# Kernel tuning notes

Measured on AMD Instinct MI355X. Metric: run time of the kernel, lower is better.

Reference implementation:

```python
import jax, jax.numpy as jnp
import numpy as np

EMBED = 1024
HEADS = 16
HEAD_DIM = 64
FF = 4096
EPS = 1e-5


def _layernorm(x, g, b):
    mu = jnp.mean(x, axis=-1, keepdims=True)
    var = jnp.mean(jnp.square(x - mu), axis=-1, keepdims=True)
    return (x - mu) * jax.lax.rsqrt(var + EPS) * g + b


def setup_inputs() -> dict:
    key = jax.random.key(0)
    ks = jax.random.split(key, 12)
    s_in = 1.0 / np.sqrt(EMBED)
    s_hd = 1.0 / np.sqrt(HEADS * HEAD_DIM)
    s_ff = 1.0 / np.sqrt(FF)
    return {
        "x": jax.random.normal(ks[0], (4, 2048, EMBED), dtype=jnp.float32),
        "Wq": jax.random.uniform(ks[1], (HEADS, EMBED, HEAD_DIM), jnp.float32, -s_in, s_in),
        "Wk": jax.random.uniform(ks[2], (HEADS, EMBED, HEAD_DIM), jnp.float32, -s_in, s_in),
        "Wv": jax.random.uniform(ks[3], (HEADS, EMBED, HEAD_DIM), jnp.float32, -s_in, s_in),
        "Wo": jax.random.uniform(ks[4], (HEADS * HEAD_DIM, EMBED), jnp.float32, -s_hd, s_hd),
        "bo": jax.random.uniform(ks[5], (EMBED,), jnp.float32, -s_hd, s_hd),
        "W1": jax.random.uniform(ks[6], (EMBED, FF), jnp.float32, -s_in, s_in),
        "b1": jax.random.uniform(ks[7], (FF,), jnp.float32, -s_in, s_in),
        "W2": jax.random.uniform(ks[8], (FF, EMBED), jnp.float32, -s_ff, s_ff),
        "b2": jax.random.uniform(ks[9], (EMBED,), jnp.float32, -s_ff, s_ff),
        "ln1_g": jnp.ones((EMBED,), jnp.float32),
        "ln1_b": jnp.zeros((EMBED,), jnp.float32),
        "ln2_g": jnp.ones((EMBED,), jnp.float32),
        "ln2_b": jnp.zeros((EMBED,), jnp.float32),
    }


def reference(x, Wq, Wk, Wv, Wo, bo, W1, b1, W2, b2, ln1_g, ln1_b, ln2_g, ln2_b):
    B, T, C = x.shape
    h = _layernorm(x, ln1_g, ln1_b)
    # per-head projections, batched over heads: [B,H,T,Dh]
    q = jnp.einsum("btc,hcd->bhtd", h, Wq)
    k = jnp.einsum("btc,hcd->bhtd", h, Wk)
    v = jnp.einsum("btc,hcd->bhtd", h, Wv)
    scale = HEAD_DIM ** -0.5
    att = jnp.einsum("bhtd,bhsd->bhts", q, k) * scale  # [B,H,T,T]
    causal = jnp.tril(jnp.ones((T, T), dtype=bool))
    att = jnp.where(causal, att, -jnp.inf)
    att = jax.nn.softmax(att, axis=-1)
    out = jnp.einsum("bhts,bhsd->bhtd", att, v)  # [B,H,T,Dh]
    # concat heads (matches torch.cat over head outputs) -> [B,T,H*Dh]
    out = out.transpose(0, 2, 1, 3).reshape(B, T, HEADS * HEAD_DIM)
    x = x + out @ Wo + bo
    h2 = _layernorm(x, ln2_g, ln2_b)
    ff = jax.nn.relu(h2 @ W1 + b1) @ W2 + b2
    return x + ff
```

## Files before the change

### kernel.cpp

```cpp
#include <hip/hip_runtime.h>
#include <hip/hip_bf16.h>

#define EMBED 1024
#define HEADS 16
#define HEAD_DIM 64
#define FFDIM 4096
#define TSEQ 2048
#define BATCH 4
#define ROWS (BATCH * TSEQ)

typedef __bf16 bf16;
typedef __attribute__((ext_vector_type(8))) __bf16 bf16x8;
typedef __attribute__((ext_vector_type(4))) __bf16 bf16x4;
typedef __attribute__((ext_vector_type(4))) float f32x4;

typedef const __attribute__((address_space(1))) void* gvp;
typedef __attribute__((address_space(3))) void* svp;

__global__ __launch_bounds__(256) void conv_wqkv_t(
    const float* __restrict__ Wq, const float* __restrict__ Wk,
    const float* __restrict__ Wv, bf16* __restrict__ WqkvT) {
  __shared__ bf16 t[64][72];
  int tid = threadIdx.x;
  int k0 = blockIdx.x * 64;
  int head = blockIdx.y;
  int which = blockIdx.z;
  const float* src = which == 0 ? Wq : which == 1 ? Wk : Wv;
  float scale = which == 0 ? 0.125f * 1.44269504088896f : 1.0f;
  src += (size_t)head * 65536;
  bf16* dst = WqkvT + ((size_t)which * 1024 + head * 64) * 1024;
#pragma unroll
  for (int i = 0; i < 4; ++i) {
    int r = i * 16 + (tid >> 4);
    int c = (tid & 15) * 4;
    float4 v = *(const float4*)&src[(size_t)(k0 + r) * 64 + c];
    t[c + 0][r] = (bf16)(v.x * scale);
    t[c + 1][r] = (bf16)(v.y * scale);
    t[c + 2][r] = (bf16)(v.z * scale);
    t[c + 3][r] = (bf16)(v.w * scale);
  }
  __syncthreads();
#pragma unroll
  for (int i = 0; i < 2; ++i) {
    int r = i * 32 + (tid >> 3);
    int c = (tid & 7) * 8;
    bf16x8 o;
#pragma unroll
    for (int j = 0; j < 8; ++j) o[j] = t[r][c + j];
    *(bf16x8*)&dst[(size_t)r * 1024 + k0 + c] = o;
  }
}

__global__ __launch_bounds__(256) void transpose_conv(
    const float* __restrict__ W, bf16* __restrict__ WT, int K, int N) {
  __shared__ bf16 t[64][72];
  int tid = threadIdx.x;
  int n0 = blockIdx.x * 64, k0 = blockIdx.y * 64;
#pragma unroll
  for (int i = 0; i < 4; ++i) {
    int r = i * 16 + (tid >> 4);
    int c = (tid & 15) * 4;
    float4 v = *(const float4*)&W[(size_t)(k0 + r) * N + n0 + c];
    t[c + 0][r] = (bf16)v.x;
    t[c + 1][r] = (bf16)v.y;
    t[c + 2][r] = (bf16)v.z;
    t[c + 3][r] = (bf16)v.w;
  }
  __syncthreads();
#pragma unroll
  for (int i = 0; i < 2; ++i) {
    int r = i * 32 + (tid >> 3);
    int c = (tid & 7) * 8;
    bf16x8 o;
#pragma unroll
    for (int j = 0; j < 8; ++j) o[j] = t[r][c + j];
    *(bf16x8*)&WT[(size_t)(n0 + r) * K + k0 + c] = o;
  }
}

__global__ __launch_bounds__(256) void transpose_v(const bf16* __restrict__ v,
                                                   bf16* __restrict__ vt) {
  __shared__ bf16 t[64][72];
  int bh = blockIdx.y;
  int t0 = blockIdx.x * 64;
  const bf16* src = v + (size_t)bh * 131072;
  bf16* dst = vt + (size_t)bh * 131072;
  int tid = threadIdx.x;
#pragma unroll
  for (int i = 0; i < 2; ++i) {
    int c = tid + i * 256;
    int r = c >> 3, d0 = (c & 7) * 8;
    bf16x8 vv = *(const bf16x8*)&src[(size_t)(t0 + r) * 64 + d0];
#pragma unroll
    for (int j = 0; j < 8; ++j) t[d0 + j][r] = vv[j];
  }
  __syncthreads();
#pragma unroll
  for (int i = 0; i < 2; ++i) {
    int c = tid + i * 256;
    int r = c >> 3, s0 = (c & 7) * 8;
    bf16x8 o;
#pragma unroll
    for (int j = 0; j < 8; ++j) o[j] = t[r][s0 + j];
    *(bf16x8*)&dst[(size_t)r * 2048 + t0 + s0] = o;
  }
}

__global__ __launch_bounds__(256) void ln_kernel(
    const float* __restrict__ x, const float* __restrict__ g,
    const float* __restrict__ bta, bf16* __restrict__ out) {
  int row = blockIdx.x;
  const float* xr = x + (size_t)row * EMBED;
  float4 v = ((const float4*)xr)[threadIdx.x];
  float s1 = v.x + v.y + v.z + v.w;
  float s2 = v.x * v.x + v.y * v.y + v.z * v.z + v.w * v.w;
#pragma unroll
  for (int off = 1; off < 64; off <<= 1) {
    s1 += __shfl_xor(s1, off);
    s2 += __shfl_xor(s2, off);
  }
  __shared__ float red[8];
  int wid = threadIdx.x >> 6;
  int lane = threadIdx.x & 63;
  if (lane == 0) {
    red[wid * 2] = s1;
    red[wid * 2 + 1] = s2;
  }
  __syncthreads();
  s1 = red[0] + red[2] + red[4] + red[6];
  s2 = red[1] + red[3] + red[5] + red[7];
  float mu = s1 * (1.0f / EMBED);
  float var = s2 * (1.0f / EMBED) - mu * mu;
  float rs = rsqrtf(var + 1e-5f);
  float4 gv = ((const float4*)g)[threadIdx.x];
  float4 bv = ((const float4*)bta)[threadIdx.x];
  bf16x4 o;
  o[0] = (bf16)((v.x - mu) * rs * gv.x + bv.x);
  o[1] = (bf16)((v.y - mu) * rs * gv.y + bv.y);
  o[2] = (bf16)((v.z - mu) * rs * gv.z + bv.z);
  o[3] = (bf16)((v.w - mu) * rs * gv.w + bv.w);
  *(bf16x4*)(out + (size_t)row * EMBED + threadIdx.x * 4) = o;
}

template <int EPI>
__global__ __launch_bounds__(512, 1) void gemm256(
    const bf16* __restrict__ A, const bf16* __restrict__ BT,
    bf16* __restrict__ Cb, const float* __restrict__ bias, int M, int N,
    int K) {
  __shared__ __attribute__((aligned(16))) char lds[98304];
  int gx = gridDim.x;
  int nwg = gx * gridDim.y;
  int wgid = blockIdx.y * gx + blockIdx.x;
  int cpx = nwg >> 3;
  int swz = (wgid & 7) * cpx + (wgid >> 3);
  int m0 = (swz / gx) * 256, n0 = (swz % gx) * 256;
  int tid = threadIdx.x;
  int lane = tid & 63, wid = tid >> 6;
  int lr = lane & 15, lg = lane >> 4;
  int wrM = (wid >> 2) * 128;
  int wcN = (wid & 3) * 64;
  int crow = lane >> 2;
  int slotg = (lane & 3) ^ (crow & 3);
  int NT = K >> 5;
  size_t rb = (size_t)K * 2;

  auto stageA = [&](int t) {
    char* dst = lds + ((unsigned)t % 3u) * 32768u;
#pragma unroll
    for (int q = 0; q < 2; ++q) {
      int c = wid * 2 + q;
      const char* srcA = (const char*)A + (size_t)(m0 + c * 16 + crow) * rb +
                         (size_t)t * 64 + slotg * 16;
      __builtin_amdgcn_global_load_lds((gvp)srcA, (svp)(dst + c * 1024), 16, 0,
                                       0);
    }
  };
  auto stageB = [&](int t) {
    char* dst = lds + ((unsigned)t % 3u) * 32768u + 16384u;
#pragma unroll
    for (int q = 0; q < 2; ++q) {
      int c = wid * 2 + q;
      const char* srcB = (const char*)BT + (size_t)(n0 + c * 16 + crow) * rb +
                         (size_t)t * 64 + slotg * 16;
      __builtin_amdgcn_global_load_lds((gvp)srcB, (svp)(dst + c * 1024), 16, 0,
                                       0);
    }
  };

  stageA(0);
  stageB(0);
  stageA(1);
  stageB(1);
  f32x4 acc[8][4] = {};
  int swcol = ((lg ^ (lr & 3)) * 16);
  for (int t = 0; t < NT; ++t) {
    if (t == NT - 1)
      asm volatile("s_waitcnt vmcnt(0)" ::: "memory");
    else
      asm volatile("s_waitcnt vmcnt(4)" ::: "memory");
    __builtin_amdgcn_s_barrier();
    __builtin_amdgcn_sched_barrier(0);
    const char* Ab = lds + ((unsigned)t % 3u) * 32768u;
    const char* Bb = Ab + 16384;
    int tn = t + 2;
    bool st = tn < NT;
    bf16x8 bfr[4], afA[4], afB[4];
#pragma unroll
    for (int j = 0; j < 4; ++j)
      bfr[j] = *(const bf16x8*)(Bb + (wcN + j * 16 + lr) * 64 + swcol);
#pragma unroll
    for (int i = 0; i < 4; ++i)
      afA[i] = *(const bf16x8*)(Ab + (wrM + i * 16 + lr) * 64 + swcol);
    if (st) stageA(tn);
    __builtin_amdgcn_s_barrier();
    __builtin_amdgcn_sched_barrier(0);
    __builtin_amdgcn_s_setprio(1);
#pragma unroll
    for (int i = 0; i < 4; ++i)
#pragma unroll
      for (int j = 0; j < 4; ++j)
        acc[i][j] = __builtin_amdgcn_mfma_f32_16x16x32_bf16(afA[i], bfr[j],
                                                            acc[i][j], 0, 0, 0);
    __builtin_amdgcn_s_setprio(0);
    __builtin_amdgcn_sched_barrier(0);
#pragma unroll
    for (int i = 0; i < 4; ++i)
      afB[i] = *(const bf16x8*)(Ab + (wrM + 64 + i * 16 + lr) * 64 + swcol);
    if (st) stageB(tn);
    __builtin_amdgcn_s_barrier();
    __builtin_amdgcn_sched_barrier(0);
    __builtin_amdgcn_s_setprio(1);
#pragma unroll
    for (int i = 0; i < 4; ++i)
#pragma unroll
      for (int j = 0; j < 4; ++j)
        acc[4 + i][j] = __builtin_amdgcn_mfma_f32_16x16x32_bf16(
            afB[i], bfr[j], acc[4 + i][j], 0, 0, 0);
    __builtin_amdgcn_s_setprio(0);
    __builtin_amdgcn_sched_barrier(0);
  }
#pragma unroll
  for (int i = 0; i < 8; ++i) {
#pragma unroll
    for (int j = 0; j < 4; ++j) {
#pragma unroll
      for (int r = 0; r < 4; ++r) {
        int row = m0 + wrM + i * 16 + lg * 4 + r;
        int col = n0 + wcN + j * 16 + lr;
        float v = acc[i][j][r];
        if (EPI == 0) {
          int which = col >> 10, cc = col & 1023;
          int b = row >> 11, tt = row & 2047, h = cc >> 6, d = cc & 63;
          bf16* dst = Cb + (size_t)which * 8388608;
          dst[((size_t)((b << 4) + h) * TSEQ + tt) * HEAD_DIM + d] = (bf16)v;
        } else {
          size_t o = (size_t)row * N + col;
          float u = v + bias[col];
          Cb[o] = (bf16)(u > 0.f ? u : 0.f);
        }
      }
    }
  }
}

template <int EPI>
__global__ __launch_bounds__(256) void gemm_bf16(
    const bf16* __restrict__ A, const bf16* __restrict__ BT,
    float* __restrict__ Cf, bf16* __restrict__ Cb,
    const float* __restrict__ bias, const float* __restrict__ resid, int M,
    int N, int K) {
  __shared__ __attribute__((aligned(16))) bf16 As[128 * 32];
  __shared__ __attribute__((aligned(16))) bf16 Bs[128 * 32];
  int gx = gridDim.x;
  int nwg = gx * gridDim.y;
  int wgid = blockIdx.y * gx + blockIdx.x;
  int cpx = nwg >> 3;
  int swz = (wgid & 7) * cpx + (wgid >> 3);
  int m0 = (swz / gx) * 128, n0 = (swz % gx) * 128;
  int tid = threadIdx.x;
  int lane = tid & 63, wid = tid >> 6;
  int lr = lane & 15, lg = lane >> 4;
  int wr = (wid >> 1) * 64, wc = (wid & 1) * 64;
  int srow = lane >> 2;
  int sk = (lane & 3) * 8;
  f32x4 acc[4][4] = {};
  for (int kt = 0; kt < K; kt += 32) {
#pragma unroll
    for (int i = 0; i < 2; ++i) {
      int c = wid * 2 + i;
      int row = c * 16 + srow;
      const bf16* ga = &A[(size_t)(m0 + row) * K + kt + sk];
      const bf16* gb = &BT[(size_t)(n0 + row) * K + kt + sk];
      __builtin_amdgcn_global_load_lds((gvp)(const void*)ga,
                                       (svp)(void*)&As[c * 512], 16, 0, 0);
      __builtin_amdgcn_global_load_lds((gvp)(const void*)gb,
                                       (svp)(void*)&Bs[c * 512], 16, 0, 0);
    }
    __syncthreads();
    bf16x8 af[4], bfr[4];
#pragma unroll
    for (int i = 0; i < 4; ++i) {
      af[i] = *(const bf16x8*)&As[(wr + i * 16 + lr) * 32 + lg * 8];
      bfr[i] = *(const bf16x8*)&Bs[(wc + i * 16 + lr) * 32 + lg * 8];
    }
#pragma unroll
    for (int ar = 0; ar < 4; ++ar)
#pragma unroll
      for (int br = 0; br < 4; ++br)
        acc[ar][br] = __builtin_amdgcn_mfma_f32_16x16x32_bf16(
            af[ar], bfr[br], acc[ar][br], 0, 0, 0);
    __syncthreads();
  }
#pragma unroll
  for (int ar = 0; ar < 4; ++ar) {
#pragma unroll
    for (int br = 0; br < 4; ++br) {
#pragma unroll
      for (int r = 0; r < 4; ++r) {
        int row = m0 + wr + ar * 16 + lg * 4 + r;
        int col = n0 + wc + br * 16 + lr;
        float v = acc[ar][br][r];
        size_t o = (size_t)row * N + col;
        Cf[o] = resid[o] + bias[col] + v;
      }
    }
  }
}

__global__ __launch_bounds__(256) void attn_kernel(
    const bf16* __restrict__ q, const bf16* __restrict__ k,
    const bf16* __restrict__ vt, bf16* __restrict__ out) {
  __shared__ __attribute__((aligned(16))) bf16 Ks[64][68];
  __shared__ __attribute__((aligned(16))) bf16 Vs[64][68];
  __shared__ __attribute__((aligned(16))) bf16 Ps[4][32][68];
  int bh = blockIdx.x;
  int b = bh >> 4, h = bh & 15;
  const bf16* qb = q + (size_t)bh * TSEQ * HEAD_DIM;
  const bf16* kb = k + (size_t)bh * TSEQ * HEAD_DIM;
  const bf16* vb = vt + (size_t)bh * HEAD_DIM * TSEQ;
  int tid = threadIdx.x, lane = tid & 63, w = tid >> 6;
  int lr = lane & 15, lg = lane >> 4;
  int Q = 15 - blockIdx.y;
  int tw = Q * 128 + w * 32;
  bf16x8 aq[2][2];
#pragma unroll
  for (int rg = 0; rg < 2; ++rg)
#pragma unroll
    for (int kc = 0; kc < 2; ++kc)
      aq[rg][kc] = *(const bf16x8*)&qb[(size_t)(tw + rg * 16 + lr) * HEAD_DIM +
                                       kc * 32 + lg * 8];
  f32x4 o[2][4] = {};
  float lrow[2][4] = {};
  int nj = 2 * Q + 2;
  for (int j = 0; j < nj; ++j) {
#pragma unroll
    for (int i = 0; i < 2; ++i) {
      int c = tid + i * 256;
      int rr = c >> 3, ko = (c & 7) * 8;
      *(bf16x8*)&Ks[rr][ko] =
          *(const bf16x8*)&kb[(size_t)(j * 64 + rr) * HEAD_DIM + ko];
      *(bf16x8*)&Vs[rr][ko] =
          *(const bf16x8*)&vb[(size_t)rr * TSEQ + j * 64 + ko];
    }
    __syncthreads();
    f32x4 s[2][4] = {};
#pragma unroll
    for (int nb = 0; nb < 4; ++nb) {
#pragma unroll
      for (int kc = 0; kc < 2; ++kc) {
        bf16x8 bk = *(const bf16x8*)&Ks[nb * 16 + lr][kc * 32 + lg * 8];
        s[0][nb] = __builtin_amdgcn_mfma_f32_16x16x32_bf16(aq[0][kc], bk,
                                                           s[0][nb], 0, 0, 0);
        s[1][nb] = __builtin_amdgcn_mfma_f32_16x16x32_bf16(aq[1][kc], bk,
                                                           s[1][nb], 0, 0, 0);
      }
    }
    if (j >= 2 * Q) {
#pragma unroll
      for (int rg = 0; rg < 2; ++rg)
#pragma unroll
        for (int nb = 0; nb < 4; ++nb)
#pragma unroll
          for (int r = 0; r < 4; ++r) {
            int sg = j * 64 + nb * 16 + lr;
            int tg = tw + rg * 16 + lg * 4 + r;
            if (sg > tg) s[rg][nb][r] = -1e30f;
          }
    }
#pragma unroll
    for (int rg = 0; rg < 2; ++rg) {
      float p[4][4];
#pragma unroll
      for (int r = 0; r < 4; ++r) {
        float su = 0.f;
#pragma unroll
        for (int nb = 0; nb < 4; ++nb) {
          p[nb][r] = exp2f(s[rg][nb][r] - 8.0f);
          su += p[nb][r];
        }
#pragma unroll
        for (int off = 1; off < 16; off <<= 1) su += __shfl_xor(su, off);
        lrow[rg][r] += su;
      }
#pragma unroll
      for (int nb = 0; nb < 4; ++nb)
#pragma unroll
        for (int r = 0; r < 4; ++r)
          Ps[w][rg * 16 + lg * 4 + r][nb * 16 + lr] = (bf16)p[nb][r];
    }
#pragma unroll
    for (int kc = 0; kc < 2; ++kc) {
      bf16x8 pa0 = *(const bf16x8*)&Ps[w][lr][kc * 32 + lg * 8];
      bf16x8 pa1 = *(const bf16x8*)&Ps[w][16 + lr][kc * 32 + lg * 8];
#pragma unroll
      for (int br = 0; br < 4; ++br) {
        bf16x8 bv = *(const bf16x8*)&Vs[br * 16 + lr][kc * 32 + lg * 8];
        o[0][br] =
            __builtin_amdgcn_mfma_f32_16x16x32_bf16(pa0, bv, o[0][br], 0, 0, 0);
        o[1][br] =
            __builtin_amdgcn_mfma_f32_16x16x32_bf16(pa1, bv, o[1][br], 0, 0, 0);
      }
    }
    __syncthreads();
  }
#pragma unroll
  for (int rg = 0; rg < 2; ++rg)
#pragma unroll
    for (int br = 0; br < 4; ++br)
#pragma unroll
      for (int r = 0; r < 4; ++r) {
        int t = tw + rg * 16 + lg * 4 + r;
        int d = br * 16 + lr;
        float val = o[rg][br][r] / lrow[rg][r];
        out[((size_t)(b * TSEQ) + t) * EMBED + h * HEAD_DIM + d] = (bf16)val;
      }
}

extern "C" void kernel_launch(void* const* d_in, const int* in_sizes, int n_in,
                              void* d_out, int out_size, void* d_ws,
                              size_t ws_size, hipStream_t stream) {
  const float* x = (const float*)d_in[0];
  const float* Wq = (const float*)d_in[1];
  const float* Wk = (const float*)d_in[2];
  const float* Wv = (const float*)d_in[3];
  const float* Wo = (const float*)d_in[4];
  const float* bo = (const float*)d_in[5];
  const float* W1 = (const float*)d_in[6];
  const float* b1 = (const float*)d_in[7];
  const float* W2 = (const float*)d_in[8];
  const float* b2 = (const float*)d_in[9];
  const float* g1 = (const float*)d_in[10];
  const float* be1 = (const float*)d_in[11];
  const float* g2 = (const float*)d_in[12];
  const float* be2 = (const float*)d_in[13];
  float* out = (float*)d_out;
  char* ws = (char*)d_ws;

  const size_t U = 16777216;
  bf16* h = (bf16*)(ws + 0 * U);
  bf16* qb = (bf16*)(ws + 1 * U);
  bf16* vtb = (bf16*)(ws + 0 * U);
  bf16* vnb = (bf16*)(ws + 3 * U);
  bf16* ao = (bf16*)(ws + 3 * U);
  float* x1 = (float*)(ws + 4 * U);
  bf16* h2 = (bf16*)(ws + 6 * U);
  bf16* ff1 = (bf16*)(ws + 0 * U);
  char* wbase = ws + 7 * U;
  bf16* WqkvT = (bf16*)(wbase);
  bf16* WoT = (bf16*)(wbase + 6291456);
  bf16* W1T = (bf16*)(wbase + 8388608);
  bf16* W2T = (bf16*)(wbase + 16777216);

  hipLaunchKernelGGL(conv_wqkv_t, dim3(16, 16, 3), dim3(256), 0, stream, Wq,
                     Wk, Wv, WqkvT);
  hipLaunchKernelGGL(transpose_conv, dim3(16, 16), dim3(256), 0, stream, Wo,
                     WoT, 1024, 1024);
  hipLaunchKernelGGL(transpose_conv, dim3(64, 16), dim3(256), 0, stream, W1,
                     W1T, 1024, 4096);
  hipLaunchKernelGGL(transpose_conv, dim3(16, 64), dim3(256), 0, stream, W2,
                     W2T, 4096, 1024);
  hipLaunchKernelGGL(ln_kernel, dim3(8192), dim3(256), 0, stream, x, g1, be1,
                     h);
  hipLaunchKernelGGL((gemm256<0>), dim3(12, 32), dim3(512), 0, stream, h,
                     WqkvT, qb, (const float*)nullptr, ROWS, 3072, 1024);
  hipLaunchKernelGGL(transpose_v, dim3(32, 64), dim3(256), 0, stream, vnb,
                     vtb);
  hipLaunchKernelGGL(attn_kernel, dim3(64, 16), dim3(256), 0, stream, qb,
                     qb + 8388608, vtb, ao);
  hipLaunchKernelGGL((gemm_bf16<2>), dim3(8, 64), dim3(256), 0, stream, ao,
                     WoT, x1, (bf16*)nullptr, bo, x, ROWS, 1024, 1024);
  hipLaunchKernelGGL(ln_kernel, dim3(8192), dim3(256), 0, stream, x1, g2, be2,
                     h2);
  hipLaunchKernelGGL((gemm256<3>), dim3(16, 32), dim3(512), 0, stream, h2, W1T,
                     ff1, b1, ROWS, 4096, 1024);
  hipLaunchKernelGGL((gemm_bf16<2>), dim3(8, 64), dim3(256), 0, stream, ff1,
                     W2T, out, (bf16*)nullptr, b2, x1, ROWS, 1024, 4096);
}
```

Measured before the change: 458.6 us.

## Split long causal attention query blocks across two workgroups with combine pass

Result: slower. 490.0 us (+6.9%).

```diff
diff --git a/kernel.cpp b/kernel.cpp
--- a/kernel.cpp
+++ b/kernel.cpp
@@ -329,18 +329,27 @@
 
 __global__ __launch_bounds__(256) void attn_kernel(
     const bf16* __restrict__ q, const bf16* __restrict__ k,
-    const bf16* __restrict__ vt, bf16* __restrict__ out) {
+    const bf16* __restrict__ vt, bf16* __restrict__ out,
+    float* __restrict__ part) {
   __shared__ __attribute__((aligned(16))) bf16 Ks[64][68];
   __shared__ __attribute__((aligned(16))) bf16 Vs[64][68];
   __shared__ __attribute__((aligned(16))) bf16 Ps[4][32][68];
-  int bh = blockIdx.x;
+  constexpr int QA[24] = {15, 15, 7, 14, 14, 13, 13, 6, 12, 12, 11, 11,
+                          5,  10, 10, 4, 9,  9,  8,  8, 3,  2,  1,  0};
+  constexpr int J0[24] = {0, 16, 0, 0, 15, 0, 14, 0, 0, 13, 0, 12,
+                          0, 0,  11, 0, 0, 10, 0, 9, 0, 0,  0, 0};
+  constexpr int J1[24] = {16, 32, 16, 15, 30, 14, 28, 14, 13, 26, 12, 24,
+                          12, 11, 22, 10, 10, 20, 9,  18, 8,  6,  4,  2};
+  constexpr int SL[24] = {14, 15, -1, 12, 13, 10, 11, -1, 8,  9,  6,  7,
+                          -1, 4,  5,  -1, 2,  3,  0,  1,  -1, -1, -1, -1};
+  int item = blockIdx.x, bh = blockIdx.y;
+  int Q = QA[item], j0 = J0[item], j1 = J1[item], slot = SL[item];
   int b = bh >> 4, h = bh & 15;
   const bf16* qb = q + (size_t)bh * TSEQ * HEAD_DIM;
   const bf16* kb = k + (size_t)bh * TSEQ * HEAD_DIM;
   const bf16* vb = vt + (size_t)bh * HEAD_DIM * TSEQ;
   int tid = threadIdx.x, lane = tid & 63, w = tid >> 6;
   int lr = lane & 15, lg = lane >> 4;
-  int Q = 15 - blockIdx.y;
   int tw = Q * 128 + w * 32;
   bf16x8 aq[2][2];
 #pragma unroll
@@ -351,8 +360,7 @@
                                        kc * 32 + lg * 8];
   f32x4 o[2][4] = {};
   float lrow[2][4] = {};
-  int nj = 2 * Q + 2;
-  for (int j = 0; j < nj; ++j) {
+  for (int j = j0; j < j1; ++j) {
 #pragma unroll
     for (int i = 0; i < 2; ++i) {
       int c = tid + i * 256;
@@ -423,17 +431,54 @@
     }
     __syncthreads();
   }
-#pragma unroll
-  for (int rg = 0; rg < 2; ++rg)
-#pragma unroll
-    for (int br = 0; br < 4; ++br)
-#pragma unroll
-      for (int r = 0; r < 4; ++r) {
-        int t = tw + rg * 16 + lg * 4 + r;
-        int d = br * 16 + lr;
-        float val = o[rg][br][r] / lrow[rg][r];
-        out[((size_t)(b * TSEQ) + t) * EMBED + h * HEAD_DIM + d] = (bf16)val;
-      }
+  if (slot < 0) {
+#pragma unroll
+    for (int rg = 0; rg < 2; ++rg)
+#pragma unroll
+      for (int br = 0; br < 4; ++br)
+#pragma unroll
+        for (int r = 0; r < 4; ++r) {
+          int t = tw + rg * 16 + lg * 4 + r;
+          int d = br * 16 + lr;
+          float val = o[rg][br][r] / lrow[rg][r];
+          out[((size_t)(b * TSEQ) + t) * EMBED + h * HEAD_DIM + d] = (bf16)val;
+        }
+  } else {
+    float* pb = part + ((size_t)bh * 16 + slot) * 8320;
+#pragma unroll
+    for (int rg = 0; rg < 2; ++rg)
+#pragma unroll
+      for (int br = 0; br < 4; ++br)
+#pragma unroll
+        for (int r = 0; r < 4; ++r) {
+          int row = w * 32 + rg * 16 + lg * 4 + r;
+          int d = br * 16 + lr;
+          pb[row * 64 + d] = o[rg][br][r];
+        }
+    if (lr == 0) {
+#pragma unroll
+      for (int rg = 0; rg < 2; ++rg)
+#pragma unroll
+        for (int r = 0; r < 4; ++r)
+          pb[8192 + w * 32 + rg * 16 + lg * 4 + r] = lrow[rg][r];
+    }
+  }
+}
+
+__global__ __launch_bounds__(256) void combine_attn(
+    const float* __restrict__ part, bf16* __restrict__ out) {
+  int bh = blockIdx.x;
+  int Q = 8 + blockIdx.y;
+  int b = bh >> 4, h = bh & 15;
+  const float* pa = part + ((size_t)bh * 16 + (Q - 8) * 2) * 8320;
+  const float* pc = pa + 8320;
+  for (int i = threadIdx.x; i < 8192; i += 256) {
+    int row = i >> 6, d = i & 63;
+    float l = pa[8192 + row] + pc[8192 + row];
+    float v = (pa[i] + pc[i]) / l;
+    int t = Q * 128 + row;
+    out[((size_t)(b * TSEQ) + t) * EMBED + h * HEAD_DIM + d] = (bf16)v;
+  }
 }
 
 extern "C" void kernel_launch(void* const* d_in, const int* in_sizes, int n_in,
@@ -463,6 +508,7 @@
   bf16* vnb = (bf16*)(ws + 3 * U);
   bf16* ao = (bf16*)(ws + 3 * U);
   float* x1 = (float*)(ws + 4 * U);
+  float* attn_part = (float*)(ws + 4 * U);
   bf16* h2 = (bf16*)(ws + 6 * U);
   bf16* ff1 = (bf16*)(ws + 0 * U);
   char* wbase = ws + 7 * U;
@@ -485,8 +531,10 @@
                      WqkvT, qb, (const float*)nullptr, ROWS, 3072, 1024);
   hipLaunchKernelGGL(transpose_v, dim3(32, 64), dim3(256), 0, stream, vnb,
                      vtb);
-  hipLaunchKernelGGL(attn_kernel, dim3(64, 16), dim3(256), 0, stream, qb,
-                     qb + 8388608, vtb, ao);
+  hipLaunchKernelGGL(attn_kernel, dim3(24, 64), dim3(256), 0, stream, qb,
+                     qb + 8388608, vtb, ao, attn_part);
+  hipLaunchKernelGGL(combine_attn, dim3(64, 8), dim3(256), 0, stream,
+                     attn_part, ao);
   hipLaunchKernelGGL((gemm_bf16<2>), dim3(8, 64), dim3(256), 0, stream, ao,
                      WoT, x1, (bf16*)nullptr, bo, x, ROWS, 1024, 1024);
   hipLaunchKernelGGL(ln_kernel, dim3(8192), dim3(256), 0, stream, x1, g2, be2,
```
